# Kernel tuning notes

Measured on AMD Instinct MI355X. Metric: run time of the kernel, lower is better.

Reference implementation:

```python
import jax, jax.numpy as jnp
import numpy as np

BLOCK = 128
NUM_LEVELS = 16  # 2**num_bits, num_bits=4
FIXED_T = 100.0
EPS = 1e-6


def _blockify(w, B):
    R, C = w.shape
    # [R, C] -> [nb, B, B] with nb = (R//B)*(C//B), row-major block order
    return w.reshape(R // B, B, C // B, B).transpose(0, 2, 1, 3).reshape(-1, B, B)


def _unblockify(blocks, R, C, B):
    return blocks.reshape(R // B, C // B, B, B).transpose(0, 2, 1, 3).reshape(R, C)


def setup_inputs() -> dict:
    key = jax.random.key(0)
    R, C = 4096, 4096
    weight = jax.random.normal(key, (R, C), dtype=jnp.float32)
    blocks = _blockify(weight, BLOCK)
    w_min = blocks.min(axis=(1, 2))  # [nb]
    w_max = blocks.max(axis=(1, 2))  # [nb]
    return {"weight": weight, "w_min": w_min, "w_max": w_max}


def reference(weight, w_min, w_max):
    R, C = weight.shape
    blocks = _blockify(weight, BLOCK)  # [nb, B, B]

    # clamp semantics of the torch code: w_min clamped against detached original
    # w_max; w_max clamped against detached *clamped* w_min (via .item()).
    wmin = jnp.minimum(w_min, jax.lax.stop_gradient(w_max) - EPS)
    wmax = jnp.maximum(w_max, jax.lax.stop_gradient(wmin) + EPS)
    wmin = wmin[:, None, None]
    wmax = wmax[:, None, None]

    scale = wmax - wmin + EPS
    w_norm = (blocks - wmin) / scale                      # [nb, B, B]
    levels = jnp.linspace(0.0, 1.0, NUM_LEVELS, dtype=weight.dtype)  # [L]
    dists = -jnp.abs(w_norm[..., None] - levels)           # [nb, B, B, L]
    soft_probs = jax.nn.softmax(dists * FIXED_T, axis=-1)  # [nb, B, B, L]
    w_q = jnp.sum(soft_probs * levels, axis=-1)            # [nb, B, B]
    w_deq = w_q * (wmax - wmin) + wmin

    # Faithful to torch: sum over dim 0 of each block (its rows) -> [nb, B, L]
    bin_mass = soft_probs.sum(axis=1)
    bin_probs = bin_mass / (bin_mass.sum(axis=(1, 2), keepdims=True) + EPS)
    total_entropy = -jnp.sum(bin_probs * jnp.log(bin_probs + EPS))

    out = _unblockify(w_deq, R, C, BLOCK)
    return out, total_entropy
```

## Files before the change

kernel.cpp:

```cpp
#include <hip/hip_runtime.h>

#define EPS 1e-6f

static constexpr float C2  = 9.617966939259756f;
static constexpr float GC  = 1.2742546176474651e-3f;
static constexpr float C3  = 0.9987273661986602f;
static constexpr float D1  = 511.0f * C3;

typedef float floatx4 __attribute__((ext_vector_type(4)));

#if __has_builtin(__builtin_amdgcn_exp2f)
__device__ __forceinline__ float fast_exp2(float x) { return __builtin_amdgcn_exp2f(x); }
#else
__device__ __forceinline__ float fast_exp2(float x) { return exp2f(x); }
#endif

#if __has_builtin(__builtin_amdgcn_rcpf)
__device__ __forceinline__ float fast_rcp(float x) { return __builtin_amdgcn_rcpf(x); }
#else
__device__ __forceinline__ float fast_rcp(float x) { return 1.0f / x; }
#endif

__device__ __forceinline__ float block_sum_512(float v, float* red, int slot) {
    #pragma unroll
    for (int o = 32; o > 0; o >>= 1) v += __shfl_xor(v, o, 64);
    const int t = threadIdx.x;
    __syncthreads();
    if ((t & 63) == 0) red[slot * 8 + (t >> 6)] = v;
    __syncthreads();
    float s = 0.0f;
    #pragma unroll
    for (int wv = 0; wv < 8; ++wv) s += red[slot * 8 + wv];
    return s;
}

__global__ __launch_bounds__(512, 8) void bq_main_kernel(
    const float* __restrict__ weight,
    const float* __restrict__ w_min,
    const float* __restrict__ w_max,
    float* __restrict__ out,
    float* __restrict__ ent_partial)
{
    __shared__ unsigned int bins[16 * 128];
    __shared__ float red[16];

    const int bid = blockIdx.x;
    const int br = bid >> 5;
    const int bc = bid & 31;
    const int t = threadIdx.x;
    const int cq = t & 31;
    const int rg = t >> 5;

    #pragma unroll
    for (int i = 0; i < 4; ++i) bins[t + i * 512] = 0u;

    const float wmn = w_min[bid];
    const float wmx = w_max[bid];
    const float lo = fminf(wmn, wmx - EPS);
    const float hi = fmaxf(wmx, lo + EPS);
    const float scale = hi - lo + EPS;
    const float s15 = 15.0f / scale;
    const float dmm15 = (hi - lo) * (1.0f / 15.0f);
    const float tb0 = -lo * s15;
    const float A1 = dmm15;
    const float A2 = dmm15 * (1.0f + 2.0f * GC);
    const float A3 = lo - GC * dmm15;

    __syncthreads();

    const size_t base = (size_t)(br * 128 + rg * 8) * 4096 + (size_t)(bc * 128 + cq * 4);
    const floatx4* __restrict__ wp = (const floatx4*)(weight + base);
    floatx4* __restrict__ op = (floatx4*)(out + base);

    #define PROC(K) do {                                                        \
        const float th = fmaf(w4[K], s15, tb0);                                 \
        const float nf = fminf(fmaxf(floorf(th), 0.0f), 15.0f);                 \
        const int   n  = (int)nf;                                               \
        const float f  = th - nf;                                               \
        const float z  = fast_exp2(fmaf(-2.0f * C2, f, C2));      \
        const float phi = fast_rcp(1.0f + z);                   \
        o4[K] = fmaf(nf, A1, fmaf(phi, A2, A3));                                \
        const unsigned int vi = (unsigned int)fmaf(phi, D1, 0.5f);              \
        atomicAdd(&bins[n * 128 + (K << 5) + cq], vi * 65535u + 510u);          \
    } while (0)

    #pragma unroll
    for (int i = 0; i < 8; ++i) {
        const floatx4 w4 = wp[(size_t)i * 1024];
        floatx4 o4;
        PROC(0); PROC(1); PROC(2); PROC(3);
        op[(size_t)i * 1024] = o4;
    }
    #undef PROC

    __syncthreads();

    float s_local = 0.0f, ent = 0.0f;
    float bin[16];
    if (t < 128) {
        unsigned int prev = 0u;
        #pragma unroll
        for (int j = 0; j < 16; ++j) {
            const unsigned int cur = bins[j * 128 + t];
            bin[j] = (float)((cur & 0xFFFFu) + (prev >> 16));
            prev = cur;
            s_local += bin[j];
        }
    }

    const float B = block_sum_512(s_local, red, 0);
    const float invB = fast_rcp(B + EPS);

    if (t < 128) {
        #pragma unroll
        for (int j = 0; j < 16; ++j) {
            const float p = bin[j] * invB;
            ent = fmaf(p, __logf(p + EPS), ent);
        }
    }
    const float entB = block_sum_512(ent, red, 1);
    if (t == 0) ent_partial[bid] = -entB;
}

__global__ __launch_bounds__(64) void bq_ent_reduce(
    const float* __restrict__ part, float* __restrict__ out_ent)
{
    const int t = threadIdx.x;
    float v = 0.0f;
    #pragma unroll
    for (int i = 0; i < 16; ++i) v += part[t + i * 64];
    #pragma unroll
    for (int o = 32; o > 0; o >>= 1) v += __shfl_xor(v, o, 64);
    if (t == 0) out_ent[0] = v;
}

extern "C" void kernel_launch(void* const* d_in, const int* in_sizes, int n_in,
                              void* d_out, int out_size, void* d_ws, size_t ws_size,
                              hipStream_t stream) {
    const float* weight = (const float*)d_in[0];
    const float* wmin = (const float*)d_in[1];
    const float* wmax = (const float*)d_in[2];
    float* out = (float*)d_out;
    float* part = (float*)d_ws;

    bq_main_kernel<<<1024, 512, 0, stream>>>(weight, wmin, wmax, out, part);
    bq_ent_reduce<<<1, 64, 0, stream>>>(part, out + (out_size - 1));
}
```

Before: 30.14 us.

## Fuse entropy reduction into one block sum and prefetch weight loads two ahead

Rewrites per-block entropy algebraically as log(B) - sum(b log b)/B, so both sums are reduced in a single block-wide pass instead of two sequential reductions with barriers. It also software-pipelines the weight loads with a two-deep register prefetch. The algebraic form moves the EPS inside the log (log(b+eps) on unnormalized counts instead of log(p+eps)), which slightly changes numerics for tiny bins. The prefetch adds register pressure under the 512x8 launch bounds.

```diff
diff --git a/kernel.cpp b/kernel.cpp
--- a/kernel.cpp
+++ b/kernel.cpp
@@ -21,17 +21,20 @@
 __device__ __forceinline__ float fast_rcp(float x) { return 1.0f / x; }
 #endif
 
-__device__ __forceinline__ float block_sum_512(float v, float* red, int slot) {
+__device__ __forceinline__ float2 block_sum2_512(float2 v, float* red) {
     #pragma unroll
-    for (int o = 32; o > 0; o >>= 1) v += __shfl_xor(v, o, 64);
+    for (int o = 32; o > 0; o >>= 1) {
+        v.x += __shfl_xor(v.x, o, 64);
+        v.y += __shfl_xor(v.y, o, 64);
+    }
     const int t = threadIdx.x;
     __syncthreads();
-    if ((t & 63) == 0) red[slot * 8 + (t >> 6)] = v;
+    if ((t & 63) == 0) { red[(t >> 6)] = v.x; red[8 + (t >> 6)] = v.y; }
     __syncthreads();
-    float s = 0.0f;
+    float sx = 0.0f, sy = 0.0f;
     #pragma unroll
-    for (int wv = 0; wv < 8; ++wv) s += red[slot * 8 + wv];
-    return s;
+    for (int wv = 0; wv < 8; ++wv) { sx += red[wv]; sy += red[8 + wv]; }
+    return make_float2(sx, sy);
 }
 
 __global__ __launch_bounds__(512, 8) void bq_main_kernel(
@@ -73,7 +76,7 @@
     floatx4* __restrict__ op = (floatx4*)(out + base);
 
     #define PROC(K) do {                                                        \
-        const float th = fmaf(w4[K], s15, tb0);                                 \
+        const float th = fmaf(cur[K], s15, tb0);                                \
         const float nf = fminf(fmaxf(floorf(th), 0.0f), 15.0f);                 \
         const int   n  = (int)nf;                                               \
         const float f  = th - nf;                                               \
@@ -84,42 +87,37 @@
         atomicAdd(&bins[n * 128 + (K << 5) + cq], vi * 65535u + 510u);          \
     } while (0)
 
+    floatx4 cur = wp[0];
+    floatx4 nx1 = wp[1024];
     #pragma unroll
     for (int i = 0; i < 8; ++i) {
-        const floatx4 w4 = wp[(size_t)i * 1024];
+        floatx4 nx2;
+        if (i < 6) nx2 = wp[(size_t)(i + 2) * 1024];
         floatx4 o4;
         PROC(0); PROC(1); PROC(2); PROC(3);
         op[(size_t)i * 1024] = o4;
+        cur = nx1; nx1 = nx2;
     }
     #undef PROC
 
     __syncthreads();
 
-    float s_local = 0.0f, ent = 0.0f;
-    float bin[16];
+    float s_local = 0.0f, slg = 0.0f;
     if (t < 128) {
         unsigned int prev = 0u;
         #pragma unroll
         for (int j = 0; j < 16; ++j) {
-            const unsigned int cur = bins[j * 128 + t];
-            bin[j] = (float)((cur & 0xFFFFu) + (prev >> 16));
-            prev = cur;
-            s_local += bin[j];
+            const unsigned int cur_u = bins[j * 128 + t];
+            const float b = (float)((cur_u & 0xFFFFu) + (prev >> 16));
+            prev = cur_u;
+            s_local += b;
+            slg = fmaf(b, __logf(b + 1e-6f), slg);
         }
     }
 
-    const float B = block_sum_512(s_local, red, 0);
-    const float invB = fast_rcp(B + EPS);
-
-    if (t < 128) {
-        #pragma unroll
-        for (int j = 0; j < 16; ++j) {
-            const float p = bin[j] * invB;
-            ent = fmaf(p, __logf(p + EPS), ent);
-        }
-    }
-    const float entB = block_sum_512(ent, red, 1);
-    if (t == 0) ent_partial[bid] = -entB;
+    const float2 sb = block_sum2_512(make_float2(s_local, slg), red);
+    const float B = sb.x + EPS;
+    if (t == 0) ent_partial[bid] = __logf(B) - sb.y * fast_rcp(B);
 }
 
 __global__ __launch_bounds__(64) void bq_ent_reduce(
```

New measurement: 28.20 us. -6.4%, faster.
